# Kernel optimization log

Hardware: AMD Instinct MI355X
Metric: run time of the kernel (lower is better)

Reference implementation:

```python
import jax, jax.numpy as jnp
import numpy as np


def setup_inputs() -> dict:
    key = jax.random.key(0)
    ks = jax.random.split(key, 7)
    B, T, IN_F = 16384, 64, 48
    F = 32          # feature_size = len(INTERACTIVE_LIST)
    H = 128         # embedding_hidden_size
    TF, TH = T * F, T * H
    scale1 = 1.0 / np.sqrt(TF)
    scale2 = 1.0 / np.sqrt(TH)
    return {
        "x": jax.random.normal(ks[0], (B, T, IN_F), dtype=jnp.float32),
        "W1": jax.random.normal(ks[1], (TF, TH), dtype=jnp.float32) * scale1,
        "b1": jax.random.normal(ks[2], (TH,), dtype=jnp.float32) * scale1,
        "W2": jax.random.normal(ks[3], (TH, TF), dtype=jnp.float32) * scale2,
        "b2": jax.random.normal(ks[4], (TF,), dtype=jnp.float32) * scale2,
        "weight": jax.random.normal(ks[5], (T, F), dtype=jnp.float32),
        "bias": jax.random.normal(ks[6], (F,), dtype=jnp.float32) * (1.0 / np.sqrt(T)),
        "sample_index": jnp.arange(F, dtype=jnp.int32),
    }


def reference(x, W1, b1, W2, b2, weight, bias, sample_index):
    # x: [B, T, IN_F]; gather interactive feature columns -> [B, T, F]
    B = x.shape[0]
    T, F = weight.shape
    xs = jnp.take(x, sample_index, axis=2)            # [B, T, F]
    # pass_linear=True path: MLP on flattened time*feature vector
    h = jax.nn.relu(xs.reshape(B, T * F) @ W1 + b1)   # [B, T*H]; dropout = identity (eval)
    out = (h @ W2 + b2).reshape(B, T, F)              # [B, T, F]
    # vectorized form of the per-sample loop: sum over time of elementwise mul
    emb = jnp.einsum("btf,tf->bf", out, weight) + bias  # [B, F]
    return emb
```

## Files before the change

kernel.cpp:

```cpp
#include <hip/hip_runtime.h>
#include <hip/hip_bf16.h>

#define BATCH 16384
#define TT    64
#define INF   48
#define FF    32
#define TFD   2048
#define THD   8192

typedef __attribute__((ext_vector_type(8))) short bf16x8;
typedef __attribute__((ext_vector_type(4))) short bf16x4;
typedef __attribute__((ext_vector_type(4))) float f32x4;

__device__ inline void gload_lds16(const void* g, void* l) {
  __builtin_amdgcn_global_load_lds((const __attribute__((address_space(1))) void*)g,
                                   (__attribute__((address_space(3))) void*)l, 16, 0, 0);
}

__device__ inline f32x4 mfma16x16x16_bf16(bf16x4 a, bf16x4 b, f32x4 c) {
#if __has_builtin(__builtin_amdgcn_mfma_f32_16x16x16bf16_1k)
  return __builtin_amdgcn_mfma_f32_16x16x16bf16_1k(a, b, c, 0, 0, 0);
#else
  asm("v_mfma_f32_16x16x16_bf16 %0, %1, %2, %0" : "+v"(c) : "v"(a), "v"(b));
  return c;
#endif
}

__device__ inline short f32_to_bf16_bits(float x) {
  __hip_bfloat16 h = __float2bfloat16(x);
  return *reinterpret_cast<short*>(&h);
}


__global__ void gather_cast(const float* __restrict__ x, const int* __restrict__ sidx,
                            __hip_bfloat16* __restrict__ xs) {
  const int b = blockIdx.x;
  const float* xr = x + (size_t)b * TT * INF;
  __hip_bfloat16* o = xs + (size_t)b * TFD;
  for (int j = threadIdx.x; j < TFD; j += 256) {
    const int t = j >> 5, f = j & 31;
    o[j] = __float2bfloat16(xr[t * INF + sidx[f]]);
  }
}

__global__ void transpose_w1(const float* __restrict__ W1, __hip_bfloat16* __restrict__ W1t) {
  __shared__ float tile[64][65];
  const int k0 = blockIdx.x * 64;
  const int n0 = blockIdx.y * 64;
  const int tx = threadIdx.x & 63, ty = threadIdx.x >> 6;
  for (int r = ty; r < 64; r += 4)
    tile[r][tx] = W1[(size_t)(k0 + r) * THD + n0 + tx];
  __syncthreads();
  for (int r = ty; r < 64; r += 4)
    W1t[(size_t)(n0 + r) * TFD + k0 + tx] = __float2bfloat16(tile[tx][r]);
}

__global__ void make_w2eff(const float* __restrict__ W2, const float* __restrict__ b2,
                           const float* __restrict__ weight, const float* __restrict__ bias,
                           __hip_bfloat16* __restrict__ w2t, float* __restrict__ beff) {
  const int n = blockIdx.x * 8 + (threadIdx.x >> 5);
  const int f = threadIdx.x & 31;
  const float* wr = W2 + (size_t)n * TFD;
  float s = 0.f;
  #pragma unroll 8
  for (int t = 0; t < TT; ++t) s += wr[t * FF + f] * weight[t * FF + f];
  w2t[(size_t)f * THD + n] = __float2bfloat16(s);
  if (blockIdx.x == 0 && threadIdx.x < FF) {
    float sb = bias[f];
    for (int t = 0; t < TT; ++t) sb += b2[t * FF + f] * weight[t * FF + f];
    beff[f] = sb;
  }
}


__device__ inline void stage_tile(char* buf, const __hip_bfloat16* __restrict__ xs,
                                  const __hip_bfloat16* __restrict__ w1t,
                                  int b0, int n0, int k0, int wid, int l) {
  const int sub = l >> 3;
  const int c   = (l & 7) ^ sub;
  const int h   = c >> 2, kc = c & 3;
  const int kofs = k0 + kc * 8;
  const int r0 = wid * 8 + sub;
  const __hip_bfloat16* gx0 = xs  + (size_t)(b0 + 2 * r0 + h) * TFD + kofs;
  const __hip_bfloat16* gx1 = xs  + (size_t)(b0 + 128 + 2 * r0 + h) * TFD + kofs;
  const __hip_bfloat16* gw0 = w1t + (size_t)(n0 + 2 * r0 + h) * TFD + kofs;
  const __hip_bfloat16* gw1 = w1t + (size_t)(n0 + 128 + 2 * r0 + h) * TFD + kofs;
  char* lx = buf + wid * 1024;
  gload_lds16(gx0, lx);
  gload_lds16(gx1, lx + 8192);
  gload_lds16(gw0, lx + 16384);
  gload_lds16(gw1, lx + 16384 + 8192);
}

__global__ __launch_bounds__(512, 2) void gemm_fused(
    const __hip_bfloat16* __restrict__ xs,
    const __hip_bfloat16* __restrict__ w1t,
    const float* __restrict__ b1,
    const __hip_bfloat16* __restrict__ w2t,
    float* __restrict__ partial)
{
  __shared__ __align__(16) char lds[131072];
  const int tid = threadIdx.x;
  const int wid = tid >> 6, l = tid & 63;
  const int mq = wid >> 2, bq = wid & 3;
  const int lo = l & 15, hi = l >> 4;
  const int rl = lo >> 1;
  const int cofs = (((((lo & 1) << 2) | hi) ^ (rl & 7)) << 4);
  const int strip = blockIdx.x & 7;
  const int bt = blockIdx.x >> 3;
  const int b0 = bt * 256;

  const int xbase = ((bq << 5) + rl) * 128 + cofs;
  const int wbase = 16384 + ((mq << 6) + rl) * 128 + cofs;

  f32x4 acc2[2][4];
  #pragma unroll
  for (int fi = 0; fi < 2; ++fi)
    #pragma unroll
    for (int bi = 0; bi < 4; ++bi) { f32x4 z = {0.f,0.f,0.f,0.f}; acc2[fi][bi] = z; }

  for (int s = 0; s < 4; ++s) {
    const int n0 = strip * 1024 + s * 256;

    f32x4 acc[8][4];
    #pragma unroll
    for (int mi = 0; mi < 8; ++mi)
      #pragma unroll
      for (int bi = 0; bi < 4; ++bi) { f32x4 z = {0.f,0.f,0.f,0.f}; acc[mi][bi] = z; }

    stage_tile(lds,          xs, w1t, b0, n0, 0,  wid, l);
    stage_tile(lds + 32768,  xs, w1t, b0, n0, 32, wid, l);
    stage_tile(lds + 65536,  xs, w1t, b0, n0, 64, wid, l);
    asm volatile("s_waitcnt vmcnt(8)" ::: "memory");
    __builtin_amdgcn_sched_barrier(0);
    __builtin_amdgcn_s_barrier();
    __builtin_amdgcn_sched_barrier(0);

    for (int t = 0; t < 64; ++t) {
      const char* buf = lds + (size_t)(t & 3) * 32768;

      if (t < 61)
        stage_tile(lds + (size_t)((t + 3) & 3) * 32768, xs, w1t, b0, n0, (t + 3) * 32, wid, l);

      bf16x8 xf[4];
      #pragma unroll
      for (int bi = 0; bi < 4; ++bi)
        xf[bi] = *(const bf16x8*)(buf + xbase + (bi << 3) * 128);

      __builtin_amdgcn_s_setprio(1);
      #pragma unroll
      for (int mi = 0; mi < 8; ++mi) {
        const bf16x8 wf = *(const bf16x8*)(buf + wbase + (mi << 3) * 128);
        #pragma unroll
        for (int bi = 0; bi < 4; ++bi)
          acc[mi][bi] = __builtin_amdgcn_mfma_f32_16x16x32_bf16(wf, xf[bi], acc[mi][bi], 0, 0, 0);
      }
      __builtin_amdgcn_s_setprio(0);

      if (t < 61)       asm volatile("s_waitcnt vmcnt(8)" ::: "memory");
      else if (t == 61) asm volatile("s_waitcnt vmcnt(4)" ::: "memory");
      else if (t == 62) asm volatile("s_waitcnt vmcnt(0)" ::: "memory");
      __builtin_amdgcn_sched_barrier(0);
      __builtin_amdgcn_s_barrier();
      __builtin_amdgcn_sched_barrier(0);
    }

    #pragma unroll
    for (int mi = 0; mi < 8; ++mi) {
      const int nbase = n0 + (mq << 7) + (mi << 4);
      const float4 b1v = *(const float4*)(b1 + nbase + (hi << 2));
      bf16x4 p[4];
      #pragma unroll
      for (int bi = 0; bi < 4; ++bi) {
        bf16x4 pk;
        #pragma unroll
        for (int j = 0; j < 4; ++j) {
          float v = acc[mi][bi][j] + ((const float*)&b1v)[j];
          v = v > 0.f ? v : 0.f;
          pk[j] = f32_to_bf16_bits(v);
        }
        p[bi] = pk;
      }
      bf16x4 a2[2];
      #pragma unroll
      for (int fi = 0; fi < 2; ++fi)
        a2[fi] = *(const bf16x4*)(w2t + (size_t)(fi * 16 + lo) * THD + nbase + (hi << 2));
      #pragma unroll
      for (int fi = 0; fi < 2; ++fi)
        #pragma unroll
        for (int bi = 0; bi < 4; ++bi)
          acc2[fi][bi] = mfma16x16x16_bf16(a2[fi], p[bi], acc2[fi][bi]);
    }
  }

  float* sm = (float*)lds;
  if (mq == 1) {
    #pragma unroll
    for (int fi = 0; fi < 2; ++fi)
      #pragma unroll
      for (int bi = 0; bi < 4; ++bi)
        *(f32x4*)(sm + ((bq << 6) + (bi << 4) + lo) * 32 + fi * 16 + (hi << 2)) = acc2[fi][bi];
  }
  __syncthreads();
  if (mq == 0) {
    #pragma unroll
    for (int fi = 0; fi < 2; ++fi)
      #pragma unroll
      for (int bi = 0; bi < 4; ++bi) {
        f32x4 other = *(const f32x4*)(sm + ((bq << 6) + (bi << 4) + lo) * 32 + fi * 16 + (hi << 2));
        f32x4 v = acc2[fi][bi] + other;
        *(f32x4*)(partial + ((size_t)strip * BATCH + b0 + (bq << 6) + (bi << 4) + lo) * FF + fi * 16 + (hi << 2)) = v;
      }
  }
}

__global__ void reduce_partial(const float* __restrict__ partial, const float* __restrict__ beff,
                               float* __restrict__ out) {
  const int idx = blockIdx.x * 256 + threadIdx.x;
  float s = beff[idx & 31];
  #pragma unroll
  for (int c = 0; c < 8; ++c) s += partial[(size_t)c * BATCH * FF + idx];
  out[idx] = s;
}


extern "C" void kernel_launch(void* const* d_in, const int* in_sizes, int n_in,
                              void* d_out, int out_size, void* d_ws, size_t ws_size,
                              hipStream_t stream) {
  const float* x      = (const float*)d_in[0];
  const float* W1     = (const float*)d_in[1];
  const float* b1     = (const float*)d_in[2];
  const float* W2     = (const float*)d_in[3];
  const float* b2     = (const float*)d_in[4];
  const float* weight = (const float*)d_in[5];
  const float* bias   = (const float*)d_in[6];
  const int*   sidx   = (const int*)d_in[7];

  char* ws = (char*)d_ws;
  __hip_bfloat16* xs   = (__hip_bfloat16*)ws;
  __hip_bfloat16* w1t  = (__hip_bfloat16*)(ws + 67108864);
  __hip_bfloat16* w2t  = (__hip_bfloat16*)(ws + 100663296);
  float*          beff = (float*)(ws + 101187584);
  float*          part = (float*)(ws + 101188608);

  hipLaunchKernelGGL(gather_cast,  dim3(BATCH),   dim3(256), 0, stream, x, sidx, xs);
  hipLaunchKernelGGL(transpose_w1, dim3(32, 128), dim3(256), 0, stream, W1, w1t);
  hipLaunchKernelGGL(make_w2eff,   dim3(1024),    dim3(256), 0, stream, W2, b2, weight, bias, w2t, beff);
  hipLaunchKernelGGL(gemm_fused,   dim3(512),     dim3(512), 0, stream, xs, w1t, b1, w2t, part);
  hipLaunchKernelGGL(reduce_partial, dim3(2048),  dim3(256), 0, stream, part, beff, (float*)d_out);
}
```

Measured before the change: 625.6 us.

## Load X fragments directly to registers, stage only W1 via LDS

The fused GEMM no longer stages the activation tile through LDS. Each lane loads its X fragments from global memory straight into registers, double-buffered two k-steps ahead, and only W1 is staged via global_load_lds, which halves LDS use. The inner loop also prefetches the next W fragment pairs from LDS while the MFMAs run, and the preprocessing gather and transpose kernels now write vectorized 8- and 4-element bf16 stores. The cost is more register pressure and uncoalesced, row-strided global loads of X, plus the X reuse across warps that LDS staging provided.

```diff
diff --git a/kernel.cpp b/kernel.cpp
--- a/kernel.cpp
+++ b/kernel.cpp
@@ -10,6 +10,7 @@
 
 typedef __attribute__((ext_vector_type(8))) short bf16x8;
 typedef __attribute__((ext_vector_type(4))) short bf16x4;
+typedef __attribute__((ext_vector_type(4))) short short4v;
 typedef __attribute__((ext_vector_type(4))) float f32x4;
 
 __device__ inline void gload_lds16(const void* g, void* l) {
@@ -34,13 +35,17 @@
 
 __global__ void gather_cast(const float* __restrict__ x, const int* __restrict__ sidx,
                             __hip_bfloat16* __restrict__ xs) {
+  __shared__ int sx[FF];
+  if (threadIdx.x < FF) sx[threadIdx.x] = sidx[threadIdx.x];
+  __syncthreads();
   const int b = blockIdx.x;
-  const float* xr = x + (size_t)b * TT * INF;
-  __hip_bfloat16* o = xs + (size_t)b * TFD;
-  for (int j = threadIdx.x; j < TFD; j += 256) {
-    const int t = j >> 5, f = j & 31;
-    o[j] = __float2bfloat16(xr[t * INF + sidx[f]]);
-  }
+  const int j8 = threadIdx.x;
+  const int t = j8 >> 2, f0 = (j8 & 3) * 8;
+  const float* rowp = x + (size_t)b * TT * INF + t * INF;
+  bf16x8 v;
+  #pragma unroll
+  for (int i = 0; i < 8; ++i) v[i] = f32_to_bf16_bits(rowp[sx[f0 + i]]);
+  *(bf16x8*)(xs + (size_t)b * TFD + j8 * 8) = v;
 }
 
 __global__ void transpose_w1(const float* __restrict__ W1, __hip_bfloat16* __restrict__ W1t) {
@@ -51,8 +56,14 @@
   for (int r = ty; r < 64; r += 4)
     tile[r][tx] = W1[(size_t)(k0 + r) * THD + n0 + tx];
   __syncthreads();
-  for (int r = ty; r < 64; r += 4)
-    W1t[(size_t)(n0 + r) * TFD + k0 + tx] = __float2bfloat16(tile[tx][r]);
+  const int rn = threadIdx.x >> 4;
+  const int kq = (threadIdx.x & 15) * 4;
+  for (int rr = rn; rr < 64; rr += 16) {
+    short4v v;
+    #pragma unroll
+    for (int i = 0; i < 4; ++i) v[i] = f32_to_bf16_bits(tile[kq + i][rr]);
+    *(short4v*)(W1t + (size_t)(n0 + rr) * TFD + k0 + kq) = v;
+  }
 }
 
 __global__ void make_w2eff(const float* __restrict__ W2, const float* __restrict__ b2,
@@ -73,23 +84,57 @@
 }
 
 
-__device__ inline void stage_tile(char* buf, const __hip_bfloat16* __restrict__ xs,
-                                  const __hip_bfloat16* __restrict__ w1t,
-                                  int b0, int n0, int k0, int wid, int l) {
+__device__ inline void stage_w(char* buf, const __hip_bfloat16* __restrict__ w1t,
+                               int n0, int k0, int wid, int l) {
   const int sub = l >> 3;
   const int c   = (l & 7) ^ sub;
   const int h   = c >> 2, kc = c & 3;
-  const int kofs = k0 + kc * 8;
-  const int r0 = wid * 8 + sub;
-  const __hip_bfloat16* gx0 = xs  + (size_t)(b0 + 2 * r0 + h) * TFD + kofs;
-  const __hip_bfloat16* gx1 = xs  + (size_t)(b0 + 128 + 2 * r0 + h) * TFD + kofs;
-  const __hip_bfloat16* gw0 = w1t + (size_t)(n0 + 2 * r0 + h) * TFD + kofs;
-  const __hip_bfloat16* gw1 = w1t + (size_t)(n0 + 128 + 2 * r0 + h) * TFD + kofs;
+  const int r0  = wid * 8 + sub;
+  const __hip_bfloat16* gw0 = w1t + (size_t)(n0 + 2 * r0 + h) * TFD + k0 + kc * 8;
+  const __hip_bfloat16* gw1 = w1t + (size_t)(n0 + 128 + 2 * r0 + h) * TFD + k0 + kc * 8;
   char* lx = buf + wid * 1024;
-  gload_lds16(gx0, lx);
-  gload_lds16(gx1, lx + 8192);
-  gload_lds16(gw0, lx + 16384);
-  gload_lds16(gw1, lx + 16384 + 8192);
+  gload_lds16(gw0, lx);
+  gload_lds16(gw1, lx + 8192);
+}
+
+__device__ __forceinline__ void k_iter(char* lds, int t, int n0,
+    const __hip_bfloat16* __restrict__ xrow, const __hip_bfloat16* __restrict__ w1t,
+    f32x4 (&acc)[8][4], bf16x8 (&xfu)[4],
+    int wbase, int wid, int l) {
+  if (t <= 60) stage_w(lds + ((t + 3) & 3) * 16384, w1t, n0, (t + 3) * 32, wid, l);
+  __builtin_amdgcn_sched_barrier(0);
+  const char* buf = lds + (t & 3) * 16384;
+  bf16x8 w0  = *(const bf16x8*)(buf + wbase);
+  bf16x8 w1f = *(const bf16x8*)(buf + wbase + 1024);
+  #pragma unroll
+  for (int g = 0; g < 4; ++g) {
+    bf16x8 nw0, nw1;
+    if (g < 3) {
+      nw0 = *(const bf16x8*)(buf + wbase + (2 * g + 2) * 1024);
+      nw1 = *(const bf16x8*)(buf + wbase + (2 * g + 3) * 1024);
+    }
+    __builtin_amdgcn_s_setprio(1);
+    #pragma unroll
+    for (int bi = 0; bi < 4; ++bi)
+      acc[2 * g][bi] = __builtin_amdgcn_mfma_f32_16x16x32_bf16(w0, xfu[bi], acc[2 * g][bi], 0, 0, 0);
+    #pragma unroll
+    for (int bi = 0; bi < 4; ++bi)
+      acc[2 * g + 1][bi] = __builtin_amdgcn_mfma_f32_16x16x32_bf16(w1f, xfu[bi], acc[2 * g + 1][bi], 0, 0, 0);
+    __builtin_amdgcn_s_setprio(0);
+    if (g < 3) { w0 = nw0; w1f = nw1; }
+  }
+  if (t <= 61) {
+    #pragma unroll
+    for (int bi = 0; bi < 4; ++bi)
+      xfu[bi] = *(const bf16x8*)(xrow + (size_t)(bi << 4) * TFD + (t + 2) * 32);
+  }
+  __builtin_amdgcn_sched_barrier(0);
+  if (t <= 60)      asm volatile("s_waitcnt vmcnt(6)" ::: "memory");
+  else if (t == 61) asm volatile("s_waitcnt vmcnt(4)" ::: "memory");
+  else              asm volatile("s_waitcnt vmcnt(0)" ::: "memory");
+  __builtin_amdgcn_sched_barrier(0);
+  __builtin_amdgcn_s_barrier();
+  __builtin_amdgcn_sched_barrier(0);
 }
 
 __global__ __launch_bounds__(512, 2) void gemm_fused(
@@ -99,19 +144,19 @@
     const __hip_bfloat16* __restrict__ w2t,
     float* __restrict__ partial)
 {
-  __shared__ __align__(16) char lds[131072];
+  __shared__ __align__(16) char lds[65536];
   const int tid = threadIdx.x;
   const int wid = tid >> 6, l = tid & 63;
   const int mq = wid >> 2, bq = wid & 3;
   const int lo = l & 15, hi = l >> 4;
   const int rl = lo >> 1;
-  const int cofs = (((((lo & 1) << 2) | hi) ^ (rl & 7)) << 4);
+  const int cofs = (((((lo & 1) << 2) | hi) ^ rl) << 4);
   const int strip = blockIdx.x & 7;
   const int bt = blockIdx.x >> 3;
   const int b0 = bt * 256;
 
-  const int xbase = ((bq << 5) + rl) * 128 + cofs;
-  const int wbase = 16384 + ((mq << 6) + rl) * 128 + cofs;
+  const int wbase = ((mq << 6) + rl) * 128 + cofs;
+  const __hip_bfloat16* xrow = xs + (size_t)(b0 + (bq << 6) + lo) * TFD + (hi << 3);
 
   f32x4 acc2[2][4];
   #pragma unroll
@@ -128,41 +173,27 @@
       #pragma unroll
       for (int bi = 0; bi < 4; ++bi) { f32x4 z = {0.f,0.f,0.f,0.f}; acc[mi][bi] = z; }
 
-    stage_tile(lds,          xs, w1t, b0, n0, 0,  wid, l);
-    stage_tile(lds + 32768,  xs, w1t, b0, n0, 32, wid, l);
-    stage_tile(lds + 65536,  xs, w1t, b0, n0, 64, wid, l);
+    bf16x8 xfA[4], xfB[4];
+    stage_w(lds, w1t, n0, 0, wid, l);
+    __builtin_amdgcn_sched_barrier(0);
+    #pragma unroll
+    for (int bi = 0; bi < 4; ++bi) xfA[bi] = *(const bf16x8*)(xrow + (size_t)(bi << 4) * TFD + 0);
+    __builtin_amdgcn_sched_barrier(0);
+    stage_w(lds + 16384, w1t, n0, 32, wid, l);
+    __builtin_amdgcn_sched_barrier(0);
+    #pragma unroll
+    for (int bi = 0; bi < 4; ++bi) xfB[bi] = *(const bf16x8*)(xrow + (size_t)(bi << 4) * TFD + 32);
+    __builtin_amdgcn_sched_barrier(0);
+    stage_w(lds + 32768, w1t, n0, 64, wid, l);
+    __builtin_amdgcn_sched_barrier(0);
     asm volatile("s_waitcnt vmcnt(8)" ::: "memory");
     __builtin_amdgcn_sched_barrier(0);
     __builtin_amdgcn_s_barrier();
     __builtin_amdgcn_sched_barrier(0);
 
-    for (int t = 0; t < 64; ++t) {
-      const char* buf = lds + (size_t)(t & 3) * 32768;
-
-      if (t < 61)
-        stage_tile(lds + (size_t)((t + 3) & 3) * 32768, xs, w1t, b0, n0, (t + 3) * 32, wid, l);
-
-      bf16x8 xf[4];
-      #pragma unroll
-      for (int bi = 0; bi < 4; ++bi)
-        xf[bi] = *(const bf16x8*)(buf + xbase + (bi << 3) * 128);
-
-      __builtin_amdgcn_s_setprio(1);
-      #pragma unroll
-      for (int mi = 0; mi < 8; ++mi) {
-        const bf16x8 wf = *(const bf16x8*)(buf + wbase + (mi << 3) * 128);
-        #pragma unroll
-        for (int bi = 0; bi < 4; ++bi)
-          acc[mi][bi] = __builtin_amdgcn_mfma_f32_16x16x32_bf16(wf, xf[bi], acc[mi][bi], 0, 0, 0);
-      }
-      __builtin_amdgcn_s_setprio(0);
-
-      if (t < 61)       asm volatile("s_waitcnt vmcnt(8)" ::: "memory");
-      else if (t == 61) asm volatile("s_waitcnt vmcnt(4)" ::: "memory");
-      else if (t == 62) asm volatile("s_waitcnt vmcnt(0)" ::: "memory");
-      __builtin_amdgcn_sched_barrier(0);
-      __builtin_amdgcn_s_barrier();
-      __builtin_amdgcn_sched_barrier(0);
+    for (int tt = 0; tt < 64; tt += 2) {
+      k_iter(lds, tt,     n0, xrow, w1t, acc, xfA, wbase, wid, l);
+      k_iter(lds, tt + 1, n0, xrow, w1t, acc, xfB, wbase, wid, l);
     }
 
     #pragma unroll
```

After: 815.4 us. 30.3% more time.
